# Kernel tuning notes

Measured on AMD Instinct MI355X. Metric: run time of the kernel, lower is better.

## Reference

```python
import jax, jax.numpy as jnp
import numpy as np

EPS = 1e-12
LAMBDA = 0.5  # kernel['lambda'] for the binary kernel

D, H, Z = 3072, 1024, 32
BS, NN = 128, 32


def setup_inputs() -> dict:
    key = jax.random.key(0)
    ks = jax.random.split(key, 16)
    sc = lambda fan_in: 1.0 / np.sqrt(fan_in)
    inp = {
        "x_c": jax.random.normal(ks[0], (BS, D), jnp.float32),
        "x_nn": jax.random.normal(ks[1], (BS, NN, D), jnp.float32),
        # encoder params: D -> H -> H -> Z
        "We1": jax.random.normal(ks[2], (D, H), jnp.float32) * sc(D),
        "be1": jnp.zeros((H,), jnp.float32),
        "We2": jax.random.normal(ks[3], (H, H), jnp.float32) * sc(H),
        "be2": jnp.zeros((H,), jnp.float32),
        "We3": jax.random.normal(ks[4], (H, Z), jnp.float32) * sc(H),
        "be3": jnp.zeros((Z,), jnp.float32),
        # decoder params: Z -> H -> H -> D
        "Wd1": jax.random.normal(ks[5], (Z, H), jnp.float32) * sc(Z),
        "bd1": jnp.zeros((H,), jnp.float32),
        "Wd2": jax.random.normal(ks[6], (H, H), jnp.float32) * sc(H),
        "bd2": jnp.zeros((H,), jnp.float32),
        "Wd3": jax.random.normal(ks[7], (H, D), jnp.float32) * sc(H),
        "bd3": jnp.zeros((D,), jnp.float32),
    }
    return inp


def _mlp(x, W1, b1, W2, b2, W3, b3):
    h = jax.nn.relu(x @ W1 + b1)
    h = jax.nn.relu(h @ W2 + b2)
    return h @ W3 + b3


def reference(x_c, x_nn, We1, be1, We2, be2, We3, be3,
              Wd1, bd1, Wd2, bd2, Wd3, bd3):
    bs, num_nn, dim = x_nn.shape

    enc = lambda x: _mlp(x, We1, be1, We2, be2, We3, be3)
    dec = lambda z: _mlp(z, Wd1, bd1, Wd2, bd2, Wd3, bd3)

    z_c = enc(x_c)                                   # (bs, Z)
    z_dim = z_c.shape[1]
    z_nn = enc(x_nn.reshape(-1, dim)).reshape(bs, num_nn, z_dim)

    recon = dec(z_c)                                 # (bs, D)
    dz = z_nn - z_c[:, None, :]                      # (bs, nn, Z)
    v = dz.reshape(-1, z_dim)                        # (bs*nn, Z)
    inputs = jnp.broadcast_to(z_c[:, None, :], (bs, num_nn, z_dim)).reshape(-1, z_dim)

    # approx_order == 2: Jacobian-vector and Hessian-bilinear (dz^T H dz) via nested jvp
    jac_fn = lambda z: jax.jvp(dec, (z,), (v,))[1]   # J(z) dz, (bs*nn, D)
    jac, hess = jax.jvp(jac_fn, (inputs,), (v,))     # each (bs*nn, D)

    n_recon = recon[:, None, :] + (jac + 0.5 * hess).reshape(bs, num_nn, dim)

    n_loss = jnp.sum((x_nn - n_recon) ** 2, axis=2)  # ||.||^2, (bs, nn)

    # binary kernel: 1 where neighbor differs from center, lambda where identical
    dist = jnp.linalg.norm(x_c[:, None, :] - x_nn, axis=2)
    weights = jnp.where(dist > EPS, 1.0, LAMBDA)

    loss = jnp.mean(weights * n_loss)
    return loss
```

## Files before the change

kernel.cpp:

```cpp
#include <hip/hip_runtime.h>
#include <math.h>

#define D_DIM 3072
#define H_DIM 1024
#define Z_DIM 32
#define BATCH 128
#define NNEI 32
#define NROWS (BATCH * NNEI)
#define MENC (NROWS + BATCH)

typedef __attribute__((ext_vector_type(8))) short short8;
typedef __attribute__((ext_vector_type(4))) float f32x4;
typedef unsigned short ushortT;

__device__ __forceinline__ unsigned short f2bf(float f) {
  union { float f; unsigned int u; } v; v.f = f;
  unsigned int r = v.u + 0x7FFFu + ((v.u >> 16) & 1u);
  return (unsigned short)(r >> 16);
}
__device__ __forceinline__ float bf2f(unsigned short b) {
  union { unsigned int u; float f; } v; v.u = ((unsigned int)b) << 16;
  return v.f;
}

__device__ __forceinline__ void gl16(const ushortT* g, ushortT* l) {
  typedef __attribute__((address_space(1))) const void gvoid;
  typedef __attribute__((address_space(3))) void lvoid;
  __builtin_amdgcn_global_load_lds((gvoid*)(const void*)g, (lvoid*)(void*)l,
                                   16, 0, 0);
}
typedef __attribute__((address_space(3))) const ushortT lds_cus;
__device__ __forceinline__ short8 ldsr(const ushortT* p) {
  short8 r;
  asm volatile("ds_read_b128 %0, %1" : "=v"(r) : "v"((lds_cus*)p));
  return r;
}
#define BAR() asm volatile("s_barrier" ::: "memory")
#define VM0() asm volatile("s_waitcnt vmcnt(0)" ::: "memory")
#define LGKM0() asm volatile("s_waitcnt lgkmcnt(0)" ::: "memory")

template <int N>
__device__ __forceinline__ void vmw() {
  if constexpr (N == 0)      asm volatile("s_waitcnt vmcnt(0)" ::: "memory");
  else if constexpr (N == 2) asm volatile("s_waitcnt vmcnt(2)" ::: "memory");
  else if constexpr (N == 3) asm volatile("s_waitcnt vmcnt(3)" ::: "memory");
  else if constexpr (N == 4) asm volatile("s_waitcnt vmcnt(4)" ::: "memory");
}

enum { EP_RELU = 0, EP_BIAS = 1, EP_PART = 2, EP_LOSS = 3, EP_MASK1 = 4 };

template <int MODE, int TN>
__global__ __launch_bounds__(256) __attribute__((amdgpu_waves_per_eu(3)))
void gemm32(
    const ushortT* __restrict__ A, const ushortT* __restrict__ BT,
    const float* __restrict__ bias, ushortT* __restrict__ C,
    float* __restrict__ P, int M, int N, int K, int Ks,
    const ushortT* __restrict__ xa,
    const float* __restrict__ wrow,
    float* __restrict__ out) {
  constexpr int NF = TN / 32;

  __shared__ __align__(16) ushortT As[3][4096];
  __shared__ __align__(16) ushortT Bs[3][TN * 32];

  const int t = threadIdx.x;
  const int wave = t >> 6;
  const int lane = t & 63;
  const int quad = lane >> 4;
  const int lm = lane & 15;

  int id = blockIdx.y * gridDim.x + blockIdx.x;
  const int nwg = gridDim.x * gridDim.y;
  if ((nwg & 7) == 0) id = (id & 7) * (nwg >> 3) + (id >> 3);
  const int bm = (id / gridDim.x) * 128;
  const int bn = (id % gridDim.x) * TN;

  const int koff = blockIdx.z * Ks;
  const int wr = (wave >> 1) * 64;
  const int wc = (wave & 1) * (TN / 2);

  f32x4 acc[4][NF];
#pragma unroll
  for (int i = 0; i < 4; ++i)
#pragma unroll
    for (int j = 0; j < NF; ++j) acc[i][j] = (f32x4)0.f;

  const int srow = lane & 15;
  const int skq = lane >> 4;
  const ushortT* gA =
      A + (size_t)(bm + wave * 32 + srow) * K + koff + skq * 8;
  const size_t row16 = (size_t)16 * K;

  const ushortT* gB;
  if (TN == 128) {
    gB = BT + (size_t)(bn + wave * 32 + srow) * K + koff + skq * 8;
  } else if (TN == 64) {
    gB = BT + (size_t)(bn + wave * 16 + srow) * K + koff + skq * 8;
  } else {
    gB = BT + (size_t)(bn + (wave & 1) * 16 + srow) * K + koff + skq * 8;
  }

#define STAGE(kk, sl)                                           \
  {                                                             \
    const size_t o = (size_t)(kk) * 32;                         \
    ushortT* lA = &As[sl][wave * 1024];                         \
    gl16(gA + o, lA);                                           \
    gl16(gA + row16 + o, lA + 512);                             \
    if (TN == 128) {                                            \
      ushortT* lB = &Bs[sl][wave * 1024];                       \
      gl16(gB + o, lB);                                         \
      gl16(gB + row16 + o, lB + 512);                           \
    } else if (TN == 64) {                                      \
      gl16(gB + o, &Bs[sl][wave * 512]);                        \
    } else {                                                    \
      if (wave < 2) gl16(gB + o, &Bs[sl][(wave & 1) * 512]);    \
    }                                                           \
  }

  const int nk = Ks / 32;
  STAGE(0, 0);
  if (nk > 1) STAGE(1, 1);

  int sl = 0;
  int sn = 2;
  for (int t0 = 0; t0 < nk; ++t0) {
    if (t0 + 1 < nk) {
      if (TN == 128) vmw<4>();
      else if (TN == 64) vmw<3>();
      else { if (wave < 2) vmw<3>(); else vmw<2>(); }
    } else {
      vmw<0>();
    }
    BAR();
    if (t0 + 2 < nk) STAGE(t0 + 2, sn);

    const ushortT* arp = &As[sl][(wr >> 4) * 512 + lane * 8];
    const ushortT* brp = &Bs[sl][(wc >> 4) * 512 + lane * 8];
    short8 af[4], bf[NF];
#pragma unroll
    for (int mt = 0; mt < 4; ++mt) af[mt] = ldsr(arp + mt * 512);
#pragma unroll
    for (int nt = 0; nt < NF; ++nt) bf[nt] = ldsr(brp + nt * 512);
    LGKM0();
    __builtin_amdgcn_sched_barrier(0);
#pragma unroll
    for (int mt = 0; mt < 4; ++mt)
#pragma unroll
      for (int nt = 0; nt < NF; ++nt)
        acc[mt][nt] = __builtin_amdgcn_mfma_f32_16x16x32_bf16(
            af[mt], bf[nt], acc[mt][nt], 0, 0, 0);

    sl = (sl == 2) ? 0 : sl + 1;
    sn = (sn == 2) ? 0 : sn + 1;
  }
#undef STAGE

  if (MODE == EP_LOSS) {
    __shared__ float red[256];
    float lsum = 0.f;
#pragma unroll
    for (int mt = 0; mt < 4; ++mt) {
#pragma unroll
      for (int r = 0; r < 4; ++r) {
        const int row = bm + wr + mt * 16 + quad * 4 + r;
        const float w = wrow[row];
        const ushortT* xr = xa + (size_t)row * N;
        float rs = 0.f;
#pragma unroll
        for (int nt = 0; nt < NF; ++nt) {
          const int col = bn + wc + nt * 16 + lm;
          const float d = bf2f(xr[col]) - (acc[mt][nt][r] + bias[col]);
          rs = fmaf(d, d, rs);
        }
        lsum = fmaf(w, rs, lsum);
      }
    }
    __syncthreads();
    red[t] = lsum;
    __syncthreads();
    for (int st = 128; st > 0; st >>= 1) {
      if (t < st) red[t] += red[t + st];
      __syncthreads();
    }
    if (t == 0) atomicAdd(out, red[0] * (1.0f / (float)NROWS));
  } else if (MODE == EP_PART) {
#pragma unroll
    for (int mt = 0; mt < 4; ++mt)
#pragma unroll
      for (int r = 0; r < 4; ++r) {
        const int row = bm + wr + mt * 16 + quad * 4 + r;
#pragma unroll
        for (int nt = 0; nt < NF; ++nt) {
          const int col = bn + wc + nt * 16 + lm;
          P[((size_t)blockIdx.z * M + row) * N + col] = acc[mt][nt][r];
        }
      }
  } else {
#pragma unroll
    for (int mt = 0; mt < 4; ++mt)
#pragma unroll
      for (int r = 0; r < 4; ++r) {
        const int row = bm + wr + mt * 16 + quad * 4 + r;
#pragma unroll
        for (int nt = 0; nt < NF; ++nt) {
          const int col = bn + wc + nt * 16 + lm;
          float v = acc[mt][nt][r] + bias[col];
          if (MODE == EP_RELU) v = fmaxf(v, 0.f);
          C[(size_t)row * N + col] = f2bf(v);
        }
      }
  }
}

template <int MODE, int TN>
__global__ __launch_bounds__(256) void gemm_sb(
    const ushortT* __restrict__ A, const ushortT* __restrict__ BT,
    const float* __restrict__ bias, ushortT* __restrict__ C,
    int M, int N, int K,
    const ushortT* __restrict__ xa, const float* __restrict__ wrow,
    float* __restrict__ out) {
  constexpr int NF = TN / 32;
  __shared__ __align__(16) ushortT As[4096];
  __shared__ __align__(16) ushortT Bs[TN * 32];

  const int t = threadIdx.x;
  const int wave = t >> 6;
  const int lane = t & 63;
  const int quad = lane >> 4;
  const int lm = lane & 15;

  int id = blockIdx.y * gridDim.x + blockIdx.x;
  const int nwg = gridDim.x * gridDim.y;
  if ((nwg & 7) == 0) id = (id & 7) * (nwg >> 3) + (id >> 3);
  const int bm = (id / gridDim.x) * 128;
  const int bn = (id % gridDim.x) * TN;

  const int wr = (wave >> 1) * 64;
  const int wc = (wave & 1) * (TN / 2);

  const int a_r0 = (t >> 6) * 16 + (t & 15);
  const int a_q8 = ((t >> 4) & 3) * 8;
  const ushortT* ga0 = A + (size_t)(bm + a_r0) * K + a_q8;
  const ushortT* gb0 = BT + (size_t)(bn + a_r0) * K + a_q8;

  ushortT* asw = &As[wave * 512];
  ushortT* bsw = &Bs[wave * 512];
  gl16(ga0, asw);
  gl16(ga0 + (size_t)64 * K, asw + 2048);
  gl16(gb0, bsw);
  if (TN == 128) gl16(gb0 + (size_t)64 * K, bsw + 2048);
  VM0();
  BAR();

  f32x4 acc[4][NF];
#pragma unroll
  for (int i = 0; i < 4; ++i)
#pragma unroll
    for (int j = 0; j < NF; ++j) acc[i][j] = (f32x4)0.f;

  const ushortT* arp = As + (wr >> 4) * 512 + lane * 8;
  const ushortT* brp = Bs + (wc >> 4) * 512 + lane * 8;
  short8 af[4], bf[NF];
#pragma unroll
  for (int mt = 0; mt < 4; ++mt) af[mt] = ldsr(arp + mt * 512);
#pragma unroll
  for (int nt = 0; nt < NF; ++nt) bf[nt] = ldsr(brp + nt * 512);
  LGKM0();
  __builtin_amdgcn_sched_barrier(0);
#pragma unroll
  for (int mt = 0; mt < 4; ++mt)
#pragma unroll
    for (int nt = 0; nt < NF; ++nt)
      acc[mt][nt] = __builtin_amdgcn_mfma_f32_16x16x32_bf16(
          af[mt], bf[nt], acc[mt][nt], 0, 0, 0);

  f32x4 acc2[4][NF];
  if (MODE == EP_MASK1) {
#pragma unroll
    for (int i = 0; i < 4; ++i)
#pragma unroll
      for (int j = 0; j < NF; ++j) acc2[i][j] = (f32x4)0.f;
    if (bm < NROWS) {
      short8 az[4];
#pragma unroll
      for (int mt = 0; mt < 4; ++mt) {
        const int cz = NROWS + ((bm + wr + mt * 16) >> 5);
        az[mt] = *(const short8*)(A + (size_t)cz * K + ((lane >> 4) << 3));
      }
#pragma unroll
      for (int mt = 0; mt < 4; ++mt)
#pragma unroll
        for (int nt = 0; nt < NF; ++nt)
          acc2[mt][nt] = __builtin_amdgcn_mfma_f32_16x16x32_bf16(
              az[mt], bf[nt], acc2[mt][nt], 0, 0, 0);
    }
  }

  if (MODE == EP_MASK1) {
    const bool nb = (bm < NROWS);
#pragma unroll
    for (int mt = 0; mt < 4; ++mt)
#pragma unroll
      for (int r = 0; r < 4; ++r) {
        const int row = bm + wr + mt * 16 + quad * 4 + r;
#pragma unroll
        for (int nt = 0; nt < NF; ++nt) {
          const int col = bn + wc + nt * 16 + lm;
          const float v = acc[mt][nt][r] + bias[col];
          ushortT o;
          if (nb) {
            const float m = acc2[mt][nt][r] + bias[col];
            o = (m > 0.f) ? f2bf(v) : (ushortT)0;
          } else {
            o = f2bf(fmaxf(v, 0.f));
          }
          C[(size_t)row * N + col] = o;
        }
      }
  } else {
#pragma unroll
    for (int mt = 0; mt < 4; ++mt)
#pragma unroll
      for (int r = 0; r < 4; ++r) {
        const int row = bm + wr + mt * 16 + quad * 4 + r;
#pragma unroll
        for (int nt = 0; nt < NF; ++nt) {
          const int col = bn + wc + nt * 16 + lm;
          float v = acc[mt][nt][r] + bias[col];
          if (MODE == EP_RELU) v = fmaxf(v, 0.f);
          C[(size_t)row * N + col] = f2bf(v);
        }
      }
  }
}

template <int S, int RELU>
__global__ __launch_bounds__(256) void reduce_lin(
    const float* __restrict__ P, const float* __restrict__ bias,
    ushortT* __restrict__ outp, int MN, int Nmask) {
  const int i4 = (blockIdx.x * 256 + threadIdx.x) * 4;
  if (i4 >= MN) return;
  float4 s = *(const float4*)(P + i4);
#pragma unroll
  for (int k = 1; k < S; ++k) {
    const float4 q = *(const float4*)(P + (size_t)k * MN + i4);
    s.x += q.x; s.y += q.y; s.z += q.z; s.w += q.w;
  }
  const float4 b = *(const float4*)(bias + (i4 & Nmask));
  float vx = s.x + b.x, vy = s.y + b.y, vz = s.z + b.z, vw = s.w + b.w;
  if (RELU) {
    vx = fmaxf(vx, 0.f); vy = fmaxf(vy, 0.f);
    vz = fmaxf(vz, 0.f); vw = fmaxf(vw, 0.f);
  }
  ushort4 o;
  o.x = f2bf(vx); o.y = f2bf(vy); o.z = f2bf(vz); o.w = f2bf(vw);
  *(ushort4*)(outp + i4) = o;
}

template <int S>
__global__ __launch_bounds__(256) void reduce_lin_mask(
    const float* __restrict__ P, const float* __restrict__ bias,
    ushortT* __restrict__ outp, int MN , int MNfull ) {
  const int i4 = (blockIdx.x * 256 + threadIdx.x) * 4;
  if (i4 >= MN) return;
  const int r = i4 >> 10;
  const int c = i4 & 1023;
  const size_t ci = (((size_t)(NROWS + (r >> 5))) << 10) + c;
  float4 s = *(const float4*)(P + i4);
  float4 sc = *(const float4*)(P + ci);
#pragma unroll
  for (int k = 1; k < S; ++k) {
    const float4 q = *(const float4*)(P + (size_t)k * MNfull + i4);
    const float4 qc = *(const float4*)(P + (size_t)k * MNfull + ci);
    s.x += q.x; s.y += q.y; s.z += q.z; s.w += q.w;
    sc.x += qc.x; sc.y += qc.y; sc.z += qc.z; sc.w += qc.w;
  }
  const float4 b = *(const float4*)(bias + c);
  const float ux = s.x + b.x, uy = s.y + b.y, uz = s.z + b.z, uw = s.w + b.w;
  const float mx = sc.x + b.x, my = sc.y + b.y, mz = sc.z + b.z,
              mw = sc.w + b.w;
  ushort4 o;
  o.x = (mx > 0.f) ? f2bf(ux) : (ushortT)0;
  o.y = (my > 0.f) ? f2bf(uy) : (ushortT)0;
  o.z = (mz > 0.f) ? f2bf(uz) : (ushortT)0;
  o.w = (mw > 0.f) ? f2bf(uw) : (ushortT)0;
  *(ushort4*)(outp + i4) = o;
}

__global__ __launch_bounds__(256) void prep_kernel(
    const float* __restrict__ x_c, const float* __restrict__ x_nn,
    ushortT* __restrict__ A_enc, float* __restrict__ wbuf, float* __restrict__ out) {
  const int i = blockIdx.x;
  const int t = threadIdx.x;
  if (i < NROWS) {
    const float* src = x_nn + (size_t)i * D_DIM;
    const float* ctr = x_c + (size_t)(i >> 5) * D_DIM;
    ushortT* dst = A_enc + (size_t)i * D_DIM;
    float s = 0.f;
    for (int d = t * 4; d < D_DIM; d += 1024) {
      const float4 v = *(const float4*)(src + d);
      const float4 c = *(const float4*)(ctr + d);
      ushort4 o;
      o.x = f2bf(v.x); o.y = f2bf(v.y); o.z = f2bf(v.z); o.w = f2bf(v.w);
      *(ushort4*)(dst + d) = o;
      const float dx = v.x - c.x, dy = v.y - c.y, dz = v.z - c.z, dw = v.w - c.w;
      s += dx * dx + dy * dy + dz * dz + dw * dw;
    }
    __shared__ float red[256];
    red[t] = s;
    __syncthreads();
    for (int st = 128; st > 0; st >>= 1) {
      if (t < st) red[t] += red[t + st];
      __syncthreads();
    }
    if (t == 0) {
      wbuf[i] = (red[0] > 1e-24f) ? 1.0f : 0.5f;
      if (i == 0) out[0] = 0.f;
    }
  } else {
    const int r = i - NROWS;
    const float* src = x_c + (size_t)r * D_DIM;
    ushortT* dst = A_enc + (size_t)i * D_DIM;
    for (int d = t * 4; d < D_DIM; d += 1024) {
      const float4 v = *(const float4*)(src + d);
      ushort4 o;
      o.x = f2bf(v.x); o.y = f2bf(v.y); o.z = f2bf(v.z); o.w = f2bf(v.w);
      *(ushort4*)(dst + d) = o;
    }
  }
}

__global__ __launch_bounds__(256) void trans_all(
    const float* __restrict__ We1, const float* __restrict__ We2,
    const float* __restrict__ We3, const float* __restrict__ Wd1,
    const float* __restrict__ Wd2, const float* __restrict__ Wd3,
    ushortT* __restrict__ We1T, ushortT* __restrict__ We2T,
    ushortT* __restrict__ We3T, ushortT* __restrict__ Wd1T,
    ushortT* __restrict__ Wd2T, ushortT* __restrict__ Wd3T) {
  const int b = blockIdx.x;
  const float* W; ushortT* WT; int K, N, loc;
  if (b < 3072)      { W = We1; WT = We1T; K = 3072; N = 1024; loc = b; }
  else if (b < 4096) { W = We2; WT = We2T; K = 1024; N = 1024; loc = b - 3072; }
  else if (b < 4128) { W = We3; WT = We3T; K = 1024; N = 32;   loc = b - 4096; }
  else if (b < 4160) { W = Wd1; WT = Wd1T; K = 32;   N = 1024; loc = b - 4128; }
  else if (b < 5184) { W = Wd2; WT = Wd2T; K = 1024; N = 1024; loc = b - 4160; }
  else               { W = Wd3; WT = Wd3T; K = 1024; N = 3072; loc = b - 5184; }
  const int ntiles = N >> 5;
  const int n0 = (loc % ntiles) * 32;
  const int k0 = (loc / ntiles) * 32;
  __shared__ float tile[32][33];
  const int tx = threadIdx.x & 31;
  const int ty = threadIdx.x >> 5;
  for (int i = ty; i < 32; i += 8)
    tile[i][tx] = W[(size_t)(k0 + i) * N + n0 + tx];
  __syncthreads();
  const int n = threadIdx.x >> 3;
  const int kq = (threadIdx.x & 7) * 4;
  ushort4 o;
  o.x = f2bf(tile[kq + 0][n]);
  o.y = f2bf(tile[kq + 1][n]);
  o.z = f2bf(tile[kq + 2][n]);
  o.w = f2bf(tile[kq + 3][n]);
  *(ushort4*)(WT + (size_t)(n0 + n) * K + k0 + kq) = o;
}

extern "C" void kernel_launch(void* const* d_in, const int* in_sizes, int n_in,
                              void* d_out, int out_size, void* d_ws, size_t ws_size,
                              hipStream_t stream) {
  const float* x_c = (const float*)d_in[0];
  const float* x_nn = (const float*)d_in[1];
  const float* We1 = (const float*)d_in[2];
  const float* be1 = (const float*)d_in[3];
  const float* We2 = (const float*)d_in[4];
  const float* be2 = (const float*)d_in[5];
  const float* We3 = (const float*)d_in[6];
  const float* be3 = (const float*)d_in[7];
  const float* Wd1 = (const float*)d_in[8];
  const float* bd1 = (const float*)d_in[9];
  const float* Wd2 = (const float*)d_in[10];
  const float* bd2 = (const float*)d_in[11];
  const float* Wd3 = (const float*)d_in[12];
  const float* bd3 = (const float*)d_in[13];
  float* out = (float*)d_out;

  char* p = (char*)d_ws;
  auto alloc = [&](size_t bytes) {
    char* r = p;
    p += (bytes + 255) & ~(size_t)255;
    return r;
  };
  ushortT* We1T = (ushortT*)alloc((size_t)H_DIM * D_DIM * 2);
  ushortT* We2T = (ushortT*)alloc((size_t)H_DIM * H_DIM * 2);
  ushortT* We3T = (ushortT*)alloc((size_t)Z_DIM * H_DIM * 2);
  ushortT* Wd1T = (ushortT*)alloc((size_t)H_DIM * Z_DIM * 2);
  ushortT* Wd2T = (ushortT*)alloc((size_t)H_DIM * H_DIM * 2);
  ushortT* Wd3T = (ushortT*)alloc((size_t)D_DIM * H_DIM * 2);
  ushortT* A_enc = (ushortT*)alloc((size_t)MENC * D_DIM * 2);
  ushortT* bufX = (ushortT*)alloc((size_t)MENC * H_DIM * 2);
  ushortT* bufY = (ushortT*)alloc((size_t)MENC * H_DIM * 2);
  ushortT* z = (ushortT*)alloc((size_t)MENC * Z_DIM * 2);
  float* Pbig = (float*)alloc((size_t)3 * MENC * H_DIM * 4);
  float* wbuf = (float*)alloc((size_t)NROWS * 4);

  const dim3 blk(256);
  const float* nofp = nullptr;
  const ushortT* nobf = nullptr;

  prep_kernel<<<dim3(MENC), blk, 0, stream>>>(x_c, x_nn, A_enc, wbuf, out);
  trans_all<<<dim3(8256), blk, 0, stream>>>(We1, We2, We3, Wd1, Wd2, Wd3,
                                            We1T, We2T, We3T, Wd1T, Wd2T, Wd3T);

  gemm32<EP_PART, 128><<<dim3(8, 33, 3), blk, 0, stream>>>(
      A_enc, We1T, nofp, nullptr, Pbig, MENC, H_DIM, D_DIM, D_DIM / 3,
      nobf, nofp, nullptr);
  reduce_lin<3, 1><<<dim3((MENC * H_DIM) / 1024), blk, 0, stream>>>(
      Pbig, be1, bufX, MENC * H_DIM, H_DIM - 1);

  gemm32<EP_PART, 128><<<dim3(8, 33, 2), blk, 0, stream>>>(
      bufX, We2T, nofp, nullptr, Pbig, MENC, H_DIM, H_DIM, H_DIM / 2,
      nobf, nofp, nullptr);
  reduce_lin<2, 1><<<dim3((MENC * H_DIM) / 1024), blk, 0, stream>>>(
      Pbig, be2, bufY, MENC * H_DIM, H_DIM - 1);

  gemm32<EP_PART, 32><<<dim3(1, 33, 8), blk, 0, stream>>>(
      bufY, We3T, nofp, nullptr, Pbig, MENC, Z_DIM, H_DIM, H_DIM / 8,
      nobf, nofp, nullptr);
  reduce_lin<8, 0><<<dim3((MENC * Z_DIM) / 1024), blk, 0, stream>>>(
      Pbig, be3, z, MENC * Z_DIM, Z_DIM - 1);

  gemm_sb<EP_MASK1, 64><<<dim3(16, 33), blk, 0, stream>>>(
      z, Wd1T, bd1, bufY, MENC, H_DIM, Z_DIM, nobf, nofp, nullptr);
  gemm32<EP_PART, 128><<<dim3(8, 33, 2), blk, 0, stream>>>(
      bufY, Wd2T, nofp, nullptr, Pbig, MENC, H_DIM, H_DIM, H_DIM / 2,
      nobf, nofp, nullptr);
  reduce_lin_mask<2><<<dim3((NROWS * H_DIM) / 1024), blk, 0, stream>>>(
      Pbig, bd2, bufX, NROWS * H_DIM, MENC * H_DIM);
  gemm32<EP_LOSS, 128><<<dim3(24, 32, 1), blk, 0, stream>>>(
      bufX, Wd3T, bd3, nullptr, nullptr, NROWS, D_DIM, H_DIM, H_DIM,
      A_enc, wbuf, out);
}
```

Baseline: 359.0 us.

## Load GEMM fragments directly from global into registers, dropping LDS staging

Replaces the triple-buffered LDS pipeline (global_load_lds plus ds_read and barriers) with direct per-wave global loads of MFMA fragments into registers, using double-buffered register sets. The goal is to remove LDS traffic and barrier synchronisation. In exchange there is no data sharing between waves: each wave fetches its own A and B rows, so global/L2 traffic rises and the loads are strided by row, which risks poorer coalescing.

```diff
diff --git a/kernel.cpp b/kernel.cpp
--- a/kernel.cpp
+++ b/kernel.cpp
@@ -23,35 +23,11 @@
   return v.f;
 }
 
-__device__ __forceinline__ void gl16(const ushortT* g, ushortT* l) {
-  typedef __attribute__((address_space(1))) const void gvoid;
-  typedef __attribute__((address_space(3))) void lvoid;
-  __builtin_amdgcn_global_load_lds((gvoid*)(const void*)g, (lvoid*)(void*)l,
-                                   16, 0, 0);
-}
-typedef __attribute__((address_space(3))) const ushortT lds_cus;
-__device__ __forceinline__ short8 ldsr(const ushortT* p) {
-  short8 r;
-  asm volatile("ds_read_b128 %0, %1" : "=v"(r) : "v"((lds_cus*)p));
-  return r;
-}
-#define BAR() asm volatile("s_barrier" ::: "memory")
-#define VM0() asm volatile("s_waitcnt vmcnt(0)" ::: "memory")
-#define LGKM0() asm volatile("s_waitcnt lgkmcnt(0)" ::: "memory")
-
-template <int N>
-__device__ __forceinline__ void vmw() {
-  if constexpr (N == 0)      asm volatile("s_waitcnt vmcnt(0)" ::: "memory");
-  else if constexpr (N == 2) asm volatile("s_waitcnt vmcnt(2)" ::: "memory");
-  else if constexpr (N == 3) asm volatile("s_waitcnt vmcnt(3)" ::: "memory");
-  else if constexpr (N == 4) asm volatile("s_waitcnt vmcnt(4)" ::: "memory");
-}
-
 enum { EP_RELU = 0, EP_BIAS = 1, EP_PART = 2, EP_LOSS = 3, EP_MASK1 = 4 };
 
 template <int MODE, int TN>
 __global__ __launch_bounds__(256) __attribute__((amdgpu_waves_per_eu(3)))
-void gemm32(
+void gemmr(
     const ushortT* __restrict__ A, const ushortT* __restrict__ BT,
     const float* __restrict__ bias, ushortT* __restrict__ C,
     float* __restrict__ P, int M, int N, int K, int Ks,
@@ -60,9 +36,6 @@
     float* __restrict__ out) {
   constexpr int NF = TN / 32;
 
-  __shared__ __align__(16) ushortT As[3][4096];
-  __shared__ __align__(16) ushortT Bs[3][TN * 32];
-
   const int t = threadIdx.x;
   const int wave = t >> 6;
   const int lane = t & 63;
@@ -85,75 +58,44 @@
 #pragma unroll
     for (int j = 0; j < NF; ++j) acc[i][j] = (f32x4)0.f;
 
-  const int srow = lane & 15;
-  const int skq = lane >> 4;
-  const ushortT* gA =
-      A + (size_t)(bm + wave * 32 + srow) * K + koff + skq * 8;
-  const size_t row16 = (size_t)16 * K;
-
-  const ushortT* gB;
-  if (TN == 128) {
-    gB = BT + (size_t)(bn + wave * 32 + srow) * K + koff + skq * 8;
-  } else if (TN == 64) {
-    gB = BT + (size_t)(bn + wave * 16 + srow) * K + koff + skq * 8;
-  } else {
-    gB = BT + (size_t)(bn + (wave & 1) * 16 + srow) * K + koff + skq * 8;
-  }
-
-#define STAGE(kk, sl)                                           \
-  {                                                             \
-    const size_t o = (size_t)(kk) * 32;                         \
-    ushortT* lA = &As[sl][wave * 1024];                         \
-    gl16(gA + o, lA);                                           \
-    gl16(gA + row16 + o, lA + 512);                             \
-    if (TN == 128) {                                            \
-      ushortT* lB = &Bs[sl][wave * 1024];                       \
-      gl16(gB + o, lB);                                         \
-      gl16(gB + row16 + o, lB + 512);                           \
-    } else if (TN == 64) {                                      \
-      gl16(gB + o, &Bs[sl][wave * 512]);                        \
-    } else {                                                    \
-      if (wave < 2) gl16(gB + o, &Bs[sl][(wave & 1) * 512]);    \
-    }                                                           \
+  const int fr = lane & 15;
+  const int fk = (lane >> 4) * 8;
+  const ushortT* pa = A + (size_t)(bm + wr + fr) * K + koff + fk;
+  const ushortT* pb = BT + (size_t)(bn + wc + fr) * K + koff + fk;
+  const size_t r16 = (size_t)16 * K;
+
+  short8 aX[4], bX[NF], aY[4], bY[NF];
+
+#define LOADF(aa, bb, kk)                                                  \
+  {                                                                        \
+    const size_t o = (size_t)(kk) * 32;                                    \
+    _Pragma("unroll")                                                      \
+    for (int mt = 0; mt < 4; ++mt)                                         \
+      aa[mt] = *(const short8*)(pa + (size_t)mt * r16 + o);                \
+    _Pragma("unroll")                                                      \
+    for (int nt = 0; nt < NF; ++nt)                                        \
+      bb[nt] = *(const short8*)(pb + (size_t)nt * r16 + o);                \
+  }
+#define DOMFMA(aa, bb)                                                     \
+  {                                                                        \
+    _Pragma("unroll")                                                      \
+    for (int mt = 0; mt < 4; ++mt)                                         \
+      _Pragma("unroll")                                                    \
+      for (int nt = 0; nt < NF; ++nt)                                      \
+        acc[mt][nt] = __builtin_amdgcn_mfma_f32_16x16x32_bf16(             \
+            aa[mt], bb[nt], acc[mt][nt], 0, 0, 0);                         \
   }
 
   const int nk = Ks / 32;
-  STAGE(0, 0);
-  if (nk > 1) STAGE(1, 1);
-
-  int sl = 0;
-  int sn = 2;
-  for (int t0 = 0; t0 < nk; ++t0) {
-    if (t0 + 1 < nk) {
-      if (TN == 128) vmw<4>();
-      else if (TN == 64) vmw<3>();
-      else { if (wave < 2) vmw<3>(); else vmw<2>(); }
-    } else {
-      vmw<0>();
-    }
-    BAR();
-    if (t0 + 2 < nk) STAGE(t0 + 2, sn);
-
-    const ushortT* arp = &As[sl][(wr >> 4) * 512 + lane * 8];
-    const ushortT* brp = &Bs[sl][(wc >> 4) * 512 + lane * 8];
-    short8 af[4], bf[NF];
-#pragma unroll
-    for (int mt = 0; mt < 4; ++mt) af[mt] = ldsr(arp + mt * 512);
-#pragma unroll
-    for (int nt = 0; nt < NF; ++nt) bf[nt] = ldsr(brp + nt * 512);
-    LGKM0();
-    __builtin_amdgcn_sched_barrier(0);
-#pragma unroll
-    for (int mt = 0; mt < 4; ++mt)
-#pragma unroll
-      for (int nt = 0; nt < NF; ++nt)
-        acc[mt][nt] = __builtin_amdgcn_mfma_f32_16x16x32_bf16(
-            af[mt], bf[nt], acc[mt][nt], 0, 0, 0);
-
-    sl = (sl == 2) ? 0 : sl + 1;
-    sn = (sn == 2) ? 0 : sn + 1;
-  }
-#undef STAGE
+  LOADF(aX, bX, 0);
+  for (int t0 = 0; t0 < nk; t0 += 2) {
+    if (t0 + 1 < nk) LOADF(aY, bY, t0 + 1);
+    DOMFMA(aX, bX);
+    if (t0 + 2 < nk) LOADF(aX, bX, t0 + 2);
+    if (t0 + 1 < nk) DOMFMA(aY, bY);
+  }
+#undef LOADF
+#undef DOMFMA
 
   if (MODE == EP_LOSS) {
     __shared__ float red[256];
@@ -213,15 +155,13 @@
 }
 
 template <int MODE, int TN>
-__global__ __launch_bounds__(256) void gemm_sb(
+__global__ __launch_bounds__(256) void gemm_sbr(
     const ushortT* __restrict__ A, const ushortT* __restrict__ BT,
     const float* __restrict__ bias, ushortT* __restrict__ C,
     int M, int N, int K,
     const ushortT* __restrict__ xa, const float* __restrict__ wrow,
     float* __restrict__ out) {
   constexpr int NF = TN / 32;
-  __shared__ __align__(16) ushortT As[4096];
-  __shared__ __align__(16) ushortT Bs[TN * 32];
 
   const int t = threadIdx.x;
   const int wave = t >> 6;
@@ -238,35 +178,25 @@
   const int wr = (wave >> 1) * 64;
   const int wc = (wave & 1) * (TN / 2);
 
-  const int a_r0 = (t >> 6) * 16 + (t & 15);
-  const int a_q8 = ((t >> 4) & 3) * 8;
-  const ushortT* ga0 = A + (size_t)(bm + a_r0) * K + a_q8;
-  const ushortT* gb0 = BT + (size_t)(bn + a_r0) * K + a_q8;
-
-  ushortT* asw = &As[wave * 512];
-  ushortT* bsw = &Bs[wave * 512];
-  gl16(ga0, asw);
-  gl16(ga0 + (size_t)64 * K, asw + 2048);
-  gl16(gb0, bsw);
-  if (TN == 128) gl16(gb0 + (size_t)64 * K, bsw + 2048);
-  VM0();
-  BAR();
+  const int fr = lane & 15;
+  const int fk = (lane >> 4) * 8;
+  const ushortT* pa = A + (size_t)(bm + wr + fr) * K + fk;
+  const ushortT* pb = BT + (size_t)(bn + wc + fr) * K + fk;
+  const size_t r16 = (size_t)16 * K;
+
+  short8 af[4], bf[NF];
+#pragma unroll
+  for (int mt = 0; mt < 4; ++mt)
+    af[mt] = *(const short8*)(pa + (size_t)mt * r16);
+#pragma unroll
+  for (int nt = 0; nt < NF; ++nt)
+    bf[nt] = *(const short8*)(pb + (size_t)nt * r16);
 
   f32x4 acc[4][NF];
 #pragma unroll
   for (int i = 0; i < 4; ++i)
 #pragma unroll
     for (int j = 0; j < NF; ++j) acc[i][j] = (f32x4)0.f;
-
-  const ushortT* arp = As + (wr >> 4) * 512 + lane * 8;
-  const ushortT* brp = Bs + (wc >> 4) * 512 + lane * 8;
-  short8 af[4], bf[NF];
-#pragma unroll
-  for (int mt = 0; mt < 4; ++mt) af[mt] = ldsr(arp + mt * 512);
-#pragma unroll
-  for (int nt = 0; nt < NF; ++nt) bf[nt] = ldsr(brp + nt * 512);
-  LGKM0();
-  __builtin_amdgcn_sched_barrier(0);
 #pragma unroll
   for (int mt = 0; mt < 4; ++mt)
 #pragma unroll
@@ -285,7 +215,7 @@
 #pragma unroll
       for (int mt = 0; mt < 4; ++mt) {
         const int cz = NROWS + ((bm + wr + mt * 16) >> 5);
-        az[mt] = *(const short8*)(A + (size_t)cz * K + ((lane >> 4) << 3));
+        az[mt] = *(const short8*)(A + (size_t)cz * K + fk);
       }
 #pragma unroll
       for (int mt = 0; mt < 4; ++mt)
@@ -510,32 +440,32 @@
   trans_all<<<dim3(8256), blk, 0, stream>>>(We1, We2, We3, Wd1, Wd2, Wd3,
                                             We1T, We2T, We3T, Wd1T, Wd2T, Wd3T);
 
-  gemm32<EP_PART, 128><<<dim3(8, 33, 3), blk, 0, stream>>>(
+  gemmr<EP_PART, 128><<<dim3(8, 33, 3), blk, 0, stream>>>(
       A_enc, We1T, nofp, nullptr, Pbig, MENC, H_DIM, D_DIM, D_DIM / 3,
       nobf, nofp, nullptr);
   reduce_lin<3, 1><<<dim3((MENC * H_DIM) / 1024), blk, 0, stream>>>(
       Pbig, be1, bufX, MENC * H_DIM, H_DIM - 1);
 
-  gemm32<EP_PART, 128><<<dim3(8, 33, 2), blk, 0, stream>>>(
+  gemmr<EP_PART, 128><<<dim3(8, 33, 2), blk, 0, stream>>>(
       bufX, We2T, nofp, nullptr, Pbig, MENC, H_DIM, H_DIM, H_DIM / 2,
       nobf, nofp, nullptr);
   reduce_lin<2, 1><<<dim3((MENC * H_DIM) / 1024), blk, 0, stream>>>(
       Pbig, be2, bufY, MENC * H_DIM, H_DIM - 1);
 
-  gemm32<EP_PART, 32><<<dim3(1, 33, 8), blk, 0, stream>>>(
+  gemmr<EP_PART, 32><<<dim3(1, 33, 8), blk, 0, stream>>>(
       bufY, We3T, nofp, nullptr, Pbig, MENC, Z_DIM, H_DIM, H_DIM / 8,
       nobf, nofp, nullptr);
   reduce_lin<8, 0><<<dim3((MENC * Z_DIM) / 1024), blk, 0, stream>>>(
       Pbig, be3, z, MENC * Z_DIM, Z_DIM - 1);
 
-  gemm_sb<EP_MASK1, 64><<<dim3(16, 33), blk, 0, stream>>>(
+  gemm_sbr<EP_MASK1, 64><<<dim3(16, 33), blk, 0, stream>>>(
       z, Wd1T, bd1, bufY, MENC, H_DIM, Z_DIM, nobf, nofp, nullptr);
-  gemm32<EP_PART, 128><<<dim3(8, 33, 2), blk, 0, stream>>>(
+  gemmr<EP_PART, 128><<<dim3(8, 33, 2), blk, 0, stream>>>(
       bufY, Wd2T, nofp, nullptr, Pbig, MENC, H_DIM, H_DIM, H_DIM / 2,
       nobf, nofp, nullptr);
   reduce_lin_mask<2><<<dim3((NROWS * H_DIM) / 1024), blk, 0, stream>>>(
       Pbig, bd2, bufX, NROWS * H_DIM, MENC * H_DIM);
-  gemm32<EP_LOSS, 128><<<dim3(24, 32, 1), blk, 0, stream>>>(
+  gemmr<EP_LOSS, 128><<<dim3(24, 32, 1), blk, 0, stream>>>(
       bufX, Wd3T, bd3, nullptr, nullptr, NROWS, D_DIM, H_DIM, H_DIM,
       A_enc, wbuf, out);
 }
```

New measurement: 495.6 us. 1.38x slower.

## Replace triple-buffered BK=32 GEMM pipeline with single-buffer BK=128 loop

Applied to the files above, without the earlier changes.

Rewrites the main GEMM k-loop from a three-slot asynchronous global-to-LDS pipeline with 32-wide K steps into a single-buffer loop loading 128-wide K tiles, separated by two block barriers per step. This cuts barrier and waitcnt overhead per unit of K and lets the compiler schedule plain LDS reads. In exchange, global loads no longer overlap MFMA work within a block, LDS use per block grows, and the occupancy hint is lowered.

```diff
diff --git a/kernel.cpp b/kernel.cpp
--- a/kernel.cpp
+++ b/kernel.cpp
@@ -39,19 +39,11 @@
 #define VM0() asm volatile("s_waitcnt vmcnt(0)" ::: "memory")
 #define LGKM0() asm volatile("s_waitcnt lgkmcnt(0)" ::: "memory")
 
-template <int N>
-__device__ __forceinline__ void vmw() {
-  if constexpr (N == 0)      asm volatile("s_waitcnt vmcnt(0)" ::: "memory");
-  else if constexpr (N == 2) asm volatile("s_waitcnt vmcnt(2)" ::: "memory");
-  else if constexpr (N == 3) asm volatile("s_waitcnt vmcnt(3)" ::: "memory");
-  else if constexpr (N == 4) asm volatile("s_waitcnt vmcnt(4)" ::: "memory");
-}
-
 enum { EP_RELU = 0, EP_BIAS = 1, EP_PART = 2, EP_LOSS = 3, EP_MASK1 = 4 };
 
 template <int MODE, int TN>
-__global__ __launch_bounds__(256) __attribute__((amdgpu_waves_per_eu(3)))
-void gemm32(
+__global__ __launch_bounds__(256) __attribute__((amdgpu_waves_per_eu(2)))
+void gemm128(
     const ushortT* __restrict__ A, const ushortT* __restrict__ BT,
     const float* __restrict__ bias, ushortT* __restrict__ C,
     float* __restrict__ P, int M, int N, int K, int Ks,
@@ -60,8 +52,8 @@
     float* __restrict__ out) {
   constexpr int NF = TN / 32;
 
-  __shared__ __align__(16) ushortT As[3][4096];
-  __shared__ __align__(16) ushortT Bs[3][TN * 32];
+  __shared__ __align__(16) ushortT As[16384];
+  __shared__ __align__(16) ushortT Bs[TN * 128];
 
   const int t = threadIdx.x;
   const int wave = t >> 6;
@@ -86,72 +78,66 @@
     for (int j = 0; j < NF; ++j) acc[i][j] = (f32x4)0.f;
 
   const int srow = lane & 15;
-  const int skq = lane >> 4;
+  const int sk8 = (lane >> 4) * 8;
   const ushortT* gA =
-      A + (size_t)(bm + wave * 32 + srow) * K + koff + skq * 8;
-  const size_t row16 = (size_t)16 * K;
+      A + (size_t)(bm + wave * 32 + srow) * K + koff + sk8;
+  const size_t row16K = (size_t)16 * K;
 
   const ushortT* gB;
   if (TN == 128) {
-    gB = BT + (size_t)(bn + wave * 32 + srow) * K + koff + skq * 8;
+    gB = BT + (size_t)(bn + wave * 32 + srow) * K + koff + sk8;
   } else if (TN == 64) {
-    gB = BT + (size_t)(bn + wave * 16 + srow) * K + koff + skq * 8;
+    gB = BT + (size_t)(bn + wave * 16 + srow) * K + koff + sk8;
   } else {
-    gB = BT + (size_t)(bn + (wave & 1) * 16 + srow) * K + koff + skq * 8;
-  }
-
-#define STAGE(kk, sl)                                           \
-  {                                                             \
-    const size_t o = (size_t)(kk) * 32;                         \
-    ushortT* lA = &As[sl][wave * 1024];                         \
-    gl16(gA + o, lA);                                           \
-    gl16(gA + row16 + o, lA + 512);                             \
-    if (TN == 128) {                                            \
-      ushortT* lB = &Bs[sl][wave * 1024];                       \
-      gl16(gB + o, lB);                                         \
-      gl16(gB + row16 + o, lB + 512);                           \
-    } else if (TN == 64) {                                      \
-      gl16(gB + o, &Bs[sl][wave * 512]);                        \
-    } else {                                                    \
-      if (wave < 2) gl16(gB + o, &Bs[sl][(wave & 1) * 512]);    \
-    }                                                           \
-  }
-
-  const int nk = Ks / 32;
-  STAGE(0, 0);
-  if (nk > 1) STAGE(1, 1);
-
-  int sl = 0;
-  int sn = 2;
-  for (int t0 = 0; t0 < nk; ++t0) {
-    if (t0 + 1 < nk) {
-      if (TN == 128) vmw<4>();
-      else if (TN == 64) vmw<3>();
-      else { if (wave < 2) vmw<3>(); else vmw<2>(); }
-    } else {
-      vmw<0>();
-    }
-    BAR();
-    if (t0 + 2 < nk) STAGE(t0 + 2, sn);
-
-    const ushortT* arp = &As[sl][(wr >> 4) * 512 + lane * 8];
-    const ushortT* brp = &Bs[sl][(wc >> 4) * 512 + lane * 8];
-    short8 af[4], bf[NF];
-#pragma unroll
-    for (int mt = 0; mt < 4; ++mt) af[mt] = ldsr(arp + mt * 512);
-#pragma unroll
-    for (int nt = 0; nt < NF; ++nt) bf[nt] = ldsr(brp + nt * 512);
-    LGKM0();
-    __builtin_amdgcn_sched_barrier(0);
-#pragma unroll
-    for (int mt = 0; mt < 4; ++mt)
-#pragma unroll
-      for (int nt = 0; nt < NF; ++nt)
-        acc[mt][nt] = __builtin_amdgcn_mfma_f32_16x16x32_bf16(
-            af[mt], bf[nt], acc[mt][nt], 0, 0, 0);
-
-    sl = (sl == 2) ? 0 : sl + 1;
-    sn = (sn == 2) ? 0 : sn + 1;
+    gB = BT + (size_t)(bn + (wave & 1) * 16 + srow) * K + koff + sk8;
+  }
+
+#define STAGE(k0)                                                         \
+  {                                                                       \
+    const size_t o = (size_t)(k0) * 128;                                  \
+    _Pragma("unroll")                                                     \
+    for (int kh = 0; kh < 4; ++kh) {                                      \
+      gl16(gA + o + kh * 32, &As[kh * 4096 + wave * 1024]);               \
+      gl16(gA + row16K + o + kh * 32, &As[kh * 4096 + wave * 1024 + 512]);\
+      if (TN == 128) {                                                    \
+        gl16(gB + o + kh * 32, &Bs[kh * 4096 + wave * 1024]);             \
+        gl16(gB + row16K + o + kh * 32,                                   \
+             &Bs[kh * 4096 + wave * 1024 + 512]);                         \
+      } else if (TN == 64) {                                              \
+        gl16(gB + o + kh * 32, &Bs[kh * 2048 + wave * 512]);              \
+      }                                                                   \
+    }                                                                     \
+    if (TN == 32) {                                                       \
+      const int kh0 = (wave >> 1) * 2;                                    \
+      gl16(gB + o + kh0 * 32, &Bs[kh0 * 1024 + (wave & 1) * 512]);        \
+      gl16(gB + o + (kh0 + 1) * 32,                                       \
+           &Bs[(kh0 + 1) * 1024 + (wave & 1) * 512]);                     \
+    }                                                                     \
+  }
+
+  const int nk = Ks / 128;
+  for (int k0 = 0; k0 < nk; ++k0) {
+    __syncthreads();
+    STAGE(k0);
+    __syncthreads();
+#pragma unroll
+    for (int kh = 0; kh < 4; ++kh) {
+      const ushortT* arp = &As[kh * 4096 + (wr >> 4) * 512 + lane * 8];
+      const ushortT* brp =
+          &Bs[(TN == 128 ? kh * 4096 : TN == 64 ? kh * 2048 : kh * 1024) +
+              (wc >> 4) * 512 + lane * 8];
+      short8 af[4], bf[NF];
+#pragma unroll
+      for (int mt = 0; mt < 4; ++mt) af[mt] = *(const short8*)(arp + mt * 512);
+#pragma unroll
+      for (int nt = 0; nt < NF; ++nt) bf[nt] = *(const short8*)(brp + nt * 512);
+#pragma unroll
+      for (int mt = 0; mt < 4; ++mt)
+#pragma unroll
+        for (int nt = 0; nt < NF; ++nt)
+          acc[mt][nt] = __builtin_amdgcn_mfma_f32_16x16x32_bf16(
+              af[mt], bf[nt], acc[mt][nt], 0, 0, 0);
+    }
   }
 #undef STAGE
 
@@ -510,19 +496,19 @@
   trans_all<<<dim3(8256), blk, 0, stream>>>(We1, We2, We3, Wd1, Wd2, Wd3,
                                             We1T, We2T, We3T, Wd1T, Wd2T, Wd3T);
 
-  gemm32<EP_PART, 128><<<dim3(8, 33, 3), blk, 0, stream>>>(
+  gemm128<EP_PART, 128><<<dim3(8, 33, 3), blk, 0, stream>>>(
       A_enc, We1T, nofp, nullptr, Pbig, MENC, H_DIM, D_DIM, D_DIM / 3,
       nobf, nofp, nullptr);
   reduce_lin<3, 1><<<dim3((MENC * H_DIM) / 1024), blk, 0, stream>>>(
       Pbig, be1, bufX, MENC * H_DIM, H_DIM - 1);
 
-  gemm32<EP_PART, 128><<<dim3(8, 33, 2), blk, 0, stream>>>(
+  gemm128<EP_PART, 128><<<dim3(8, 33, 2), blk, 0, stream>>>(
       bufX, We2T, nofp, nullptr, Pbig, MENC, H_DIM, H_DIM, H_DIM / 2,
       nobf, nofp, nullptr);
   reduce_lin<2, 1><<<dim3((MENC * H_DIM) / 1024), blk, 0, stream>>>(
       Pbig, be2, bufY, MENC * H_DIM, H_DIM - 1);
 
-  gemm32<EP_PART, 32><<<dim3(1, 33, 8), blk, 0, stream>>>(
+  gemm128<EP_PART, 32><<<dim3(1, 33, 8), blk, 0, stream>>>(
       bufY, We3T, nofp, nullptr, Pbig, MENC, Z_DIM, H_DIM, H_DIM / 8,
       nobf, nofp, nullptr);
   reduce_lin<8, 0><<<dim3((MENC * Z_DIM) / 1024), blk, 0, stream>>>(
@@ -530,12 +516,12 @@
 
   gemm_sb<EP_MASK1, 64><<<dim3(16, 33), blk, 0, stream>>>(
       z, Wd1T, bd1, bufY, MENC, H_DIM, Z_DIM, nobf, nofp, nullptr);
-  gemm32<EP_PART, 128><<<dim3(8, 33, 2), blk, 0, stream>>>(
+  gemm128<EP_PART, 128><<<dim3(8, 33, 2), blk, 0, stream>>>(
       bufY, Wd2T, nofp, nullptr, Pbig, MENC, H_DIM, H_DIM, H_DIM / 2,
       nobf, nofp, nullptr);
   reduce_lin_mask<2><<<dim3((NROWS * H_DIM) / 1024), blk, 0, stream>>>(
       Pbig, bd2, bufX, NROWS * H_DIM, MENC * H_DIM);
-  gemm32<EP_LOSS, 128><<<dim3(24, 32, 1), blk, 0, stream>>>(
+  gemm128<EP_LOSS, 128><<<dim3(24, 32, 1), blk, 0, stream>>>(
       bufX, Wd3T, bd3, nullptr, nullptr, NROWS, D_DIM, H_DIM, H_DIM,
       A_enc, wbuf, out);
 }
```

Result: slower. 391.0 us (+8.9%).
